# Performance work log

Hardware: AMD Instinct MI355X
Metric: run time of the kernel (lower is better)

Reference implementation:

```python
import jax, jax.numpy as jnp
import numpy as np

B, L, D, H = 8, 4096, 512, 8
DK = D // H
FACTOR = 5


def setup_inputs() -> dict:
    key = jax.random.key(0)
    ks = jax.random.split(key, 11)
    s = 0.02
    w = lambda k: (jax.random.normal(k, (D, D), jnp.float32) * s)
    b = lambda k: (jax.random.normal(k, (D,), jnp.float32) * s)
    return {
        "q": jax.random.normal(ks[0], (B, L, D), jnp.float32),
        "k": jax.random.normal(ks[1], (B, L, D), jnp.float32),
        "v": jax.random.normal(ks[2], (B, L, D), jnp.float32),
        "Wq": w(ks[3]), "bq": b(ks[4]),
        "Wk": w(ks[5]), "bk": b(ks[6]),
        "Wv": w(ks[7]), "bv": b(ks[8]),
        "Wo": w(ks[9]), "bo": b(ks[10]),
    }


def _autocorrelation(q, k, v, Wq, bq, Wk, bk, Wv, bv, Wo, bo):
    # projections -> [B, H, L, DK]
    def proj(x, W, bias):
        return (x @ W + bias).reshape(B, L, H, DK).transpose(0, 2, 1, 3)

    Q = proj(q, Wq, bq)
    K = proj(k, Wk, bk)
    V = proj(v, Wv, bv)

    # FFT-based autocorrelation along length dim
    Qf = jnp.fft.rfft(Q, axis=2)
    Kf = jnp.fft.rfft(K, axis=2)
    R = jnp.fft.irfft(Qf * jnp.conj(Kf), n=L, axis=2)  # [B, H, L, DK]

    # NOTE: this repo reduces over head then LENGTH, so topk runs over channel dim
    mean_value = R.mean(axis=(1, 2))          # [B, DK]
    mean_across_batch = mean_value.mean(axis=0)  # [DK]

    top_k = max(1, min(int(FACTOR * np.log(L)), L))
    actual_k = min(top_k, DK)                  # static: 41
    _, idx = jax.lax.top_k(mean_across_batch, actual_k)  # [k] channel-indices used as delays

    weights = jax.nn.softmax(mean_value[:, idx], axis=-1)  # [B, k]

    # top-k delay aggregation: sum_i roll(V, -idx_i, axis=2) * w_i
    t = jnp.arange(L)

    def body(acc, inp):
        d, wb = inp  # scalar delay, [B] weights
        pattern = jnp.take(V, (t + d) % L, axis=2)  # circular roll by -d
        return acc + pattern * wb[:, None, None, None], None

    agg, _ = jax.lax.scan(body, jnp.zeros_like(V), (idx, weights.T))

    out = agg.transpose(0, 2, 1, 3).reshape(B, L, D) @ Wo + bo
    return out


def reference(q, k, v, Wq, bq, Wk, bk, Wv, bv, Wo, bo):
    return _autocorrelation(q, k, v, Wq, bq, Wk, bk, Wv, bv, Wo, bo)
```

## Files before the change

kernel.cpp:

```cpp
#include <hip/hip_runtime.h>
#include <hip/hip_bf16.h>

#define LL 4096
#define DD 512
#define BB 8
#define KSEL 41

typedef __attribute__((ext_vector_type(4))) float f32x4;
typedef __attribute__((ext_vector_type(8))) short short8;

__device__ __forceinline__ ushort f2bf(float x) {
  __hip_bfloat16 h = __float2bfloat16(x);
  return *reinterpret_cast<ushort*>(&h);
}

__device__ __forceinline__ void g2lds16(const void* g, void* l) {
  __builtin_amdgcn_global_load_lds(
      (const __attribute__((address_space(1))) unsigned int*)g,
      (__attribute__((address_space(3))) unsigned int*)l, 16, 0, 0);
}

__global__ __launch_bounds__(512) void k_colsum(const float* __restrict__ q,
                                                const float* __restrict__ kk,
                                                float* __restrict__ qpart,
                                                float* __restrict__ kpart) {
  int lc = blockIdx.x, b = blockIdx.y, which = blockIdx.z;
  const float* src = which ? kk : q;
  float* part = which ? kpart : qpart;
  int lane = threadIdx.x & 63, w = threadIdx.x >> 6;
  int c8 = lane * 8;
  const float* p = src + ((size_t)b * LL + (size_t)lc * 256 + w * 32) * DD + c8;
  float a0 = 0, a1 = 0, a2 = 0, a3 = 0, a4 = 0, a5 = 0, a6 = 0, a7 = 0;
#pragma unroll 8
  for (int l = 0; l < 32; ++l) {
    f32x4 x = __builtin_nontemporal_load((const f32x4*)(p + (size_t)l * DD));
    f32x4 y = __builtin_nontemporal_load((const f32x4*)(p + (size_t)l * DD + 4));
    a0 += x[0]; a1 += x[1]; a2 += x[2]; a3 += x[3];
    a4 += y[0]; a5 += y[1]; a6 += y[2]; a7 += y[3];
  }
  float* dst = &part[((size_t)b * 128 + lc * 8 + w) * DD + c8];
  f32x4 o0 = {a0, a1, a2, a3}, o1 = {a4, a5, a6, a7};
  *(f32x4*)dst = o0;
  *(f32x4*)(dst + 4) = o1;
}

__global__ __launch_bounds__(256) void k_projw(
    const float* __restrict__ qpart, const float* __restrict__ kpart,
    const float* __restrict__ Wq, const float* __restrict__ Wk,
    const float* __restrict__ bv, const float* __restrict__ Wo,
    const float* __restrict__ Wv,
    float* __restrict__ partQ, float* __restrict__ partK,
    float* __restrict__ partO, ushort* __restrict__ WT) {
  __shared__ float ss[BB][64];
  __shared__ float wv[8][512];
  int bid = blockIdx.x;
  int tid = threadIdx.x;

  if (bid < 24) {
    int jc = bid & 7, which = bid >> 3;
    int j0 = jc * 64;
    if (which == 2) {
      float a0 = 0.f, a1 = 0.f;
      for (int j = 0; j < 64; ++j) {
        float b = bv[j0 + j];
        a0 += b * Wo[(size_t)(j0 + j) * DD + tid];
        a1 += b * Wo[(size_t)(j0 + j) * DD + tid + 256];
      }
      partO[(size_t)jc * DD + tid] = a0;
      partO[(size_t)jc * DD + tid + 256] = a1;
      return;
    }
    const float* part_in = which ? kpart : qpart;
    const float* W = which ? Wk : Wq;
    for (int e = tid; e < BB * 64; e += 256) {
      int b = e >> 6, j = e & 63;
      float s = 0.f;
#pragma unroll 8
      for (int p = 0; p < 128; ++p)
        s += part_in[((size_t)b * 128 + p) * DD + j0 + j];
      ss[b][j] = s;
    }
    __syncthreads();
    float a[BB][2];
#pragma unroll
    for (int b = 0; b < BB; ++b) { a[b][0] = 0.f; a[b][1] = 0.f; }
    for (int j = 0; j < 64; ++j) {
      float w0 = W[(size_t)(j0 + j) * DD + tid];
      float w1 = W[(size_t)(j0 + j) * DD + tid + 256];
#pragma unroll
      for (int b = 0; b < BB; ++b) {
        float sv = ss[b][j];
        a[b][0] += sv * w0;
        a[b][1] += sv * w1;
      }
    }
    float* part = which ? partK : partQ;
#pragma unroll
    for (int b = 0; b < BB; ++b) {
      part[((size_t)jc * BB + b) * DD + tid] = a[b][0];
      part[((size_t)jc * BB + b) * DD + tid + 256] = a[b][1];
    }
    return;
  }

  int b2 = bid - 24;
  int cb = b2 & 1, jg = b2 >> 1;
  int c = cb * 256 + tid;
  int j0 = jg * 8;
  for (int t = tid; t < 8 * 512; t += 256)
    wv[t >> 9][t & 511] = Wv[(size_t)(j0 + (t >> 9)) * DD + (t & 511)];
  __syncthreads();
  float acc[8] = {0, 0, 0, 0, 0, 0, 0, 0};
  for (int m = 0; m < DD; ++m) {
    float wo = Wo[(size_t)m * DD + c];
#pragma unroll
    for (int j = 0; j < 8; ++j) acc[j] += wv[j][m] * wo;
  }
  ushort4 o0, o1;
  o0.x = f2bf(acc[0]); o0.y = f2bf(acc[1]); o0.z = f2bf(acc[2]); o0.w = f2bf(acc[3]);
  o1.x = f2bf(acc[4]); o1.y = f2bf(acc[5]); o1.z = f2bf(acc[6]); o1.w = f2bf(acc[7]);
  *(ushort4*)&WT[(size_t)c * DD + j0] = o0;
  *(ushort4*)&WT[(size_t)c * DD + j0 + 4] = o1;
}

__global__ __launch_bounds__(512) void k_stats2(
    const float* __restrict__ partQ, const float* __restrict__ partK,
    const float* __restrict__ partO,
    const float* __restrict__ bq, const float* __restrict__ bk,
    const float* __restrict__ bo,
    int* __restrict__ idx_out, float* __restrict__ wts_out,
    float* __restrict__ bvo_out) {
  __shared__ float Sq[BB][DD];
  __shared__ float Sk[BB][DD];
  __shared__ float mvs[BB][64];
  __shared__ float mab[64];
  __shared__ int idxs[64];
  int tid = threadIdx.x;
  float bqv = bq[tid] * (float)LL, bkv = bk[tid] * (float)LL;
#pragma unroll
  for (int b = 0; b < BB; ++b) {
    float aq = 0.f, ak = 0.f;
#pragma unroll
    for (int jc = 0; jc < 8; ++jc) {
      aq += partQ[((size_t)jc * BB + b) * DD + tid];
      ak += partK[((size_t)jc * BB + b) * DD + tid];
    }
    Sq[b][tid] = aq + bqv;
    Sk[b][tid] = ak + bkv;
  }
  {
    float ao = 0.f;
#pragma unroll
    for (int jc = 0; jc < 8; ++jc) ao += partO[(size_t)jc * DD + tid];
    bvo_out[tid] = ao + bo[tid];
  }
  __syncthreads();
  {
    int b = tid >> 6, d = tid & 63;
    float s = 0.f;
#pragma unroll
    for (int h = 0; h < 8; ++h) s += Sq[b][h * 64 + d] * Sk[b][h * 64 + d];
    mvs[b][d] = s * (1.0f / ((float)LL * 8.0f));
  }
  __syncthreads();
  if (tid < 64) {
    float s = 0.f;
#pragma unroll
    for (int b = 0; b < BB; ++b) s += mvs[b][tid];
    mab[tid] = s * 0.125f;
  }
  __syncthreads();
  if (tid < 64) {
    float x = mab[tid];
    int r = 0;
    for (int d = 0; d < 64; ++d) {
      float y = mab[d];
      r += (y > x || (y == x && d < tid)) ? 1 : 0;
    }
    if (r < KSEL) { idxs[r] = tid; idx_out[r] = tid; }
  }
  __syncthreads();
  if (tid < BB) {
    int b = tid;
    float mx = -3.4e38f;
    for (int i = 0; i < KSEL; ++i) mx = fmaxf(mx, mvs[b][idxs[i]]);
    float s = 0.f;
    for (int i = 0; i < KSEL; ++i) s += expf(mvs[b][idxs[i]] - mx);
    float inv = 1.f / s;
    for (int i = 0; i < KSEL; ++i) wts_out[b * 64 + i] = expf(mvs[b][idxs[i]] - mx) * inv;
  }
}

__global__ __launch_bounds__(256) void k_conv(const float* __restrict__ v,
                                              const int* __restrict__ idx,
                                              const float* __restrict__ wts,
                                              ushort* __restrict__ vagg) {
  __shared__ ushort vwinT[128 * 136];
  __shared__ ushort Mlds[64 * 136];
  __shared__ float coefw[256];
  int lt = blockIdx.x;
  int ch0 = blockIdx.y * 128;
  int b = blockIdx.z;
  int tid = threadIdx.x;
  int l0 = lt * 64;

  coefw[tid] = 0.f;
  __syncthreads();
  if (tid < KSEL) coefw[64 + idx[tid]] = wts[b * 64 + tid];
  __syncthreads();

  {
    int c = tid & 127;
    int jh = tid >> 7;
    const float* vb = v + (size_t)b * LL * DD + ch0 + c;
#pragma unroll
    for (int it = 0; it < 8; ++it) {
      int j0 = (it * 2 + jh) * 8;
      union { unsigned int u[4]; short8 s; } pk;
#pragma unroll
      for (int p = 0; p < 4; ++p) {
        int ja = (l0 + j0 + 2 * p) & (LL - 1);
        int jb = (l0 + j0 + 2 * p + 1) & (LL - 1);
        float lo = vb[(size_t)ja * DD];
        float hi = vb[(size_t)jb * DD];
        pk.u[p] = (unsigned)f2bf(lo) | ((unsigned)f2bf(hi) << 16);
      }
      *(short8*)&vwinT[c * 136 + j0] = pk.s;
    }
  }
#pragma unroll
  for (int it = 0; it < 8; ++it) {
    int e = (it * 256 + tid) * 4;
    int r = e >> 7, j0 = e & 127;
    ushort4 m4;
    m4.x = f2bf(coefw[64 + j0 + 0 - r]);
    m4.y = f2bf(coefw[64 + j0 + 1 - r]);
    m4.z = f2bf(coefw[64 + j0 + 2 - r]);
    m4.w = f2bf(coefw[64 + j0 + 3 - r]);
    *(ushort4*)&Mlds[r * 136 + j0] = m4;
  }
  __syncthreads();

  int lane = tid & 63, w = tid >> 6;
  int r15 = lane & 15, g = lane >> 4;
  f32x4 acc[4][2] = {};
#pragma unroll
  for (int ks = 0; ks < 4; ++ks) {
    int kc = ks * 4 + g;
    short8 av[4], bvv[2];
#pragma unroll
    for (int m = 0; m < 4; ++m)
      av[m] = *(const short8*)&Mlds[(m * 16 + r15) * 136 + kc * 8];
#pragma unroll
    for (int n = 0; n < 2; ++n)
      bvv[n] = *(const short8*)&vwinT[(w * 32 + n * 16 + r15) * 136 + kc * 8];
#pragma unroll
    for (int m = 0; m < 4; ++m)
#pragma unroll
      for (int n = 0; n < 2; ++n)
        acc[m][n] = __builtin_amdgcn_mfma_f32_16x16x32_bf16(av[m], bvv[n], acc[m][n], 0, 0, 0);
  }

  ushort* vout = vagg + ((size_t)b * LL + l0) * DD + ch0;
#pragma unroll
  for (int m = 0; m < 4; ++m)
#pragma unroll
    for (int n = 0; n < 2; ++n)
#pragma unroll
      for (int r = 0; r < 4; ++r) {
        int row = m * 16 + g * 4 + r;
        int col = w * 32 + n * 16 + r15;
        vout[(size_t)row * DD + col] = f2bf(acc[m][n][r]);
      }
}

__global__ __launch_bounds__(256) void k_gemm(const ushort* __restrict__ A,
                                              const ushort* __restrict__ BT,
                                              const float* __restrict__ bias,
                                              float* __restrict__ C) {
  __shared__ ushort lA[128 * 64];
  __shared__ ushort lB[128 * 64];
  int bcol = blockIdx.x * 128;
  int brow = blockIdx.y * 128;
  int tid = threadIdx.x;
  int lane = tid & 63, wid = tid >> 6;
  int wr = wid >> 1, wc = wid & 1;
  int r15 = lane & 15, g = lane >> 4;
  f32x4 acc[4][4] = {};
  for (int k0 = 0; k0 < DD; k0 += 64) {
#pragma unroll
    for (int it = 0; it < 4; ++it) {
      int ch = it * 256 + tid;
      int row = ch >> 3;
      int clg = (ch & 7) ^ (row & 7);
      g2lds16(A + (size_t)(brow + row) * DD + k0 + clg * 8, &lA[ch * 8]);
      g2lds16(BT + (size_t)(bcol + row) * DD + k0 + clg * 8, &lB[ch * 8]);
    }
    asm volatile("s_waitcnt vmcnt(0)" ::: "memory");
    __syncthreads();
#pragma unroll
    for (int ks = 0; ks < 2; ++ks) {
      int kc = ks * 4 + g;
      short8 av[4], bv[4];
#pragma unroll
      for (int m = 0; m < 4; ++m) {
        int row = wr * 64 + m * 16 + r15;
        av[m] = *(const short8*)&lA[(row * 8 + (kc ^ (row & 7))) * 8];
        int col = wc * 64 + m * 16 + r15;
        bv[m] = *(const short8*)&lB[(col * 8 + (kc ^ (col & 7))) * 8];
      }
#pragma unroll
      for (int m = 0; m < 4; ++m)
#pragma unroll
        for (int n = 0; n < 4; ++n)
          acc[m][n] = __builtin_amdgcn_mfma_f32_16x16x32_bf16(av[m], bv[n], acc[m][n], 0, 0, 0);
    }
    __syncthreads();
  }
#pragma unroll
  for (int n = 0; n < 4; ++n) {
    int col = bcol + wc * 64 + n * 16 + r15;
    float bc = bias[col];
#pragma unroll
    for (int m = 0; m < 4; ++m) {
      int row = brow + wr * 64 + m * 16 + g * 4;
#pragma unroll
      for (int r = 0; r < 4; ++r)
        C[(size_t)(row + r) * DD + col] = acc[m][n][r] + bc;
    }
  }
}

extern "C" void kernel_launch(void* const* d_in, const int* in_sizes, int n_in,
                              void* d_out, int out_size, void* d_ws, size_t ws_size,
                              hipStream_t stream) {
  const float* q  = (const float*)d_in[0];
  const float* k  = (const float*)d_in[1];
  const float* v  = (const float*)d_in[2];
  const float* Wq = (const float*)d_in[3];
  const float* bq = (const float*)d_in[4];
  const float* Wk = (const float*)d_in[5];
  const float* bk = (const float*)d_in[6];
  const float* Wv = (const float*)d_in[7];
  const float* bv = (const float*)d_in[8];
  const float* Wo = (const float*)d_in[9];
  const float* bo = (const float*)d_in[10];
  float* out = (float*)d_out;

  char* ws = (char*)d_ws;
  ushort* vagg  = (ushort*)(ws + 0x0);
  ushort* wvot  = (ushort*)(ws + 0x2100000);
  int*   idx    = (int*)(ws + 0x2388800);
  float* wts    = (float*)(ws + 0x2388900);
  float* bvo    = (float*)(ws + 0x2389100);
  float* qpart  = (float*)(ws + 0x0);
  float* kpart  = (float*)(ws + 0x200000);
  float* partQ  = (float*)(ws + 0x2180000);
  float* partK  = (float*)(ws + 0x21A0000);
  float* partO  = (float*)(ws + 0x21C0000);

  k_colsum<<<dim3(16, 8, 2), 512, 0, stream>>>(q, k, qpart, kpart);
  k_projw<<<dim3(152), 256, 0, stream>>>(qpart, kpart, Wq, Wk, bv, Wo, Wv,
                                         partQ, partK, partO, wvot);
  k_stats2<<<dim3(1), 512, 0, stream>>>(partQ, partK, partO, bq, bk, bo, idx, wts, bvo);
  k_conv<<<dim3(64, 4, 8), 256, 0, stream>>>(v, idx, wts, vagg);
  k_gemm<<<dim3(4, 256), 256, 0, stream>>>(vagg, wvot, bvo, out);
}
```

Baseline: 129.1 us.

## Project V by WvWo before delay aggregation and fuse with column sums

Uses the fact that the circular delay aggregation is linear, so it commutes with the per-row projection. The projection V·(Wv·Wo) now runs first as a bf16 MFMA GEMM, fused into one launch with the q/k column-sum blocks. The shift-and-weight convolution then works on the projected bf16 P and writes the final fp32 output with the bias, which removes the separate output GEMM and the vagg round-trip. The trade-off is an extra bf16 intermediate P that must be written and re-read, and the column-sum layout changes to 32 partials per batch.

```diff
diff --git a/kernel.cpp b/kernel.cpp
--- a/kernel.cpp
+++ b/kernel.cpp
@@ -20,16 +20,116 @@
       (__attribute__((address_space(3))) unsigned int*)l, 16, 0, 0);
 }
 
-__global__ __launch_bounds__(512) void k_colsum(const float* __restrict__ q,
-                                                const float* __restrict__ kk,
-                                                float* __restrict__ qpart,
-                                                float* __restrict__ kpart) {
-  int lc = blockIdx.x, b = blockIdx.y, which = blockIdx.z;
+__global__ __launch_bounds__(256) void k_wvot(const float* __restrict__ Wv,
+                                              const float* __restrict__ Wo,
+                                              ushort* __restrict__ WT) {
+  __shared__ float wv[8][512];
+  int tid = threadIdx.x;
+  int c = blockIdx.x * 256 + tid;
+  int j0 = blockIdx.y * 8;
+  for (int t = tid; t < 8 * 512; t += 256)
+    wv[t >> 9][t & 511] = Wv[(size_t)(j0 + (t >> 9)) * DD + (t & 511)];
+  __syncthreads();
+  float acc[8] = {0, 0, 0, 0, 0, 0, 0, 0};
+  for (int m = 0; m < DD; ++m) {
+    float wo = Wo[(size_t)m * DD + c];
+#pragma unroll
+    for (int j = 0; j < 8; ++j) acc[j] += wv[j][m] * wo;
+  }
+  ushort4 o0, o1;
+  o0.x = f2bf(acc[0]); o0.y = f2bf(acc[1]); o0.z = f2bf(acc[2]); o0.w = f2bf(acc[3]);
+  o1.x = f2bf(acc[4]); o1.y = f2bf(acc[5]); o1.z = f2bf(acc[6]); o1.w = f2bf(acc[7]);
+  *(ushort4*)&WT[(size_t)c * DD + j0] = o0;
+  *(ushort4*)&WT[(size_t)c * DD + j0 + 4] = o1;
+}
+
+union SmemF {
+  struct { ushort lA[128 * 64]; ushort lB[128 * 64]; } g;
+  float red[4][512];
+};
+
+__global__ __launch_bounds__(256) void k_fused(
+    const float* __restrict__ q, const float* __restrict__ kk,
+    const float* __restrict__ v, const ushort* __restrict__ WvoT,
+    ushort* __restrict__ P, float* __restrict__ qpart, float* __restrict__ kpart) {
+  __shared__ SmemF sm;
+  int bid = blockIdx.x;
+  int tid = threadIdx.x;
+
+  if (bid < 1024) {
+    int bcol = (bid & 3) * 128;
+    int brow = ((bid >> 2) & 31) * 128;
+    int b = bid >> 7;
+    const float* vb = v + (size_t)b * LL * DD;
+    int lane = tid & 63, wid = tid >> 6;
+    int wr = wid >> 1, wc = wid & 1;
+    int r15 = lane & 15, g = lane >> 4;
+    f32x4 acc[4][4] = {};
+    for (int k0 = 0; k0 < DD; k0 += 64) {
+#pragma unroll
+      for (int it = 0; it < 4; ++it) {
+        int e = it * 256 + tid;
+        int row = e >> 3, chl = e & 7;
+        const float* src = vb + (size_t)(brow + row) * DD + k0 + ((chl ^ (row & 7)) * 8);
+        f32x4 x = *(const f32x4*)src;
+        f32x4 y = *(const f32x4*)(src + 4);
+        union { ushort us[8]; short8 s; } pk;
+        pk.us[0] = f2bf(x[0]); pk.us[1] = f2bf(x[1]);
+        pk.us[2] = f2bf(x[2]); pk.us[3] = f2bf(x[3]);
+        pk.us[4] = f2bf(y[0]); pk.us[5] = f2bf(y[1]);
+        pk.us[6] = f2bf(y[2]); pk.us[7] = f2bf(y[3]);
+        *(short8*)&sm.g.lA[e * 8] = pk.s;
+      }
+#pragma unroll
+      for (int it = 0; it < 4; ++it) {
+        int ch = it * 256 + tid;
+        int row = ch >> 3;
+        int clg = (ch & 7) ^ (row & 7);
+        g2lds16(WvoT + (size_t)(bcol + row) * DD + k0 + clg * 8, &sm.g.lB[ch * 8]);
+      }
+      asm volatile("s_waitcnt vmcnt(0)" ::: "memory");
+      __syncthreads();
+#pragma unroll
+      for (int ks = 0; ks < 2; ++ks) {
+        int kc = ks * 4 + g;
+        short8 av[4], bv[4];
+#pragma unroll
+        for (int m = 0; m < 4; ++m) {
+          int row = wr * 64 + m * 16 + r15;
+          av[m] = *(const short8*)&sm.g.lA[(row * 8 + (kc ^ (row & 7))) * 8];
+          int col = wc * 64 + m * 16 + r15;
+          bv[m] = *(const short8*)&sm.g.lB[(col * 8 + (kc ^ (col & 7))) * 8];
+        }
+#pragma unroll
+        for (int m = 0; m < 4; ++m)
+#pragma unroll
+          for (int n = 0; n < 4; ++n)
+            acc[m][n] = __builtin_amdgcn_mfma_f32_16x16x32_bf16(av[m], bv[n], acc[m][n], 0, 0, 0);
+      }
+      __syncthreads();
+    }
+    ushort* Pb = P + ((size_t)b * LL + brow) * DD + bcol;
+#pragma unroll
+    for (int n = 0; n < 4; ++n) {
+      int col = wc * 64 + n * 16 + r15;
+#pragma unroll
+      for (int m = 0; m < 4; ++m) {
+        int row = wr * 64 + m * 16 + g * 4;
+#pragma unroll
+        for (int r = 0; r < 4; ++r)
+          Pb[(size_t)(row + r) * DD + col] = f2bf(acc[m][n][r]);
+      }
+    }
+    return;
+  }
+
+  int cbid = bid - 1024;
+  int which = cbid & 1, lc = (cbid >> 1) & 31, b = cbid >> 6;
   const float* src = which ? kk : q;
   float* part = which ? kpart : qpart;
-  int lane = threadIdx.x & 63, w = threadIdx.x >> 6;
+  int lane = tid & 63, w = tid >> 6;
   int c8 = lane * 8;
-  const float* p = src + ((size_t)b * LL + (size_t)lc * 256 + w * 32) * DD + c8;
+  const float* p = src + ((size_t)b * LL + (size_t)lc * 128 + w * 32) * DD + c8;
   float a0 = 0, a1 = 0, a2 = 0, a3 = 0, a4 = 0, a5 = 0, a6 = 0, a7 = 0;
 #pragma unroll 8
   for (int l = 0; l < 32; ++l) {
@@ -38,89 +138,70 @@
     a0 += x[0]; a1 += x[1]; a2 += x[2]; a3 += x[3];
     a4 += y[0]; a5 += y[1]; a6 += y[2]; a7 += y[3];
   }
-  float* dst = &part[((size_t)b * 128 + lc * 8 + w) * DD + c8];
   f32x4 o0 = {a0, a1, a2, a3}, o1 = {a4, a5, a6, a7};
-  *(f32x4*)dst = o0;
-  *(f32x4*)(dst + 4) = o1;
-}
-
-__global__ __launch_bounds__(256) void k_projw(
+  *(f32x4*)&sm.red[w][c8] = o0;
+  *(f32x4*)&sm.red[w][c8 + 4] = o1;
+  __syncthreads();
+#pragma unroll
+  for (int t = 0; t < 2; ++t) {
+    int c = tid * 2 + t;
+    float s = sm.red[0][c] + sm.red[1][c] + sm.red[2][c] + sm.red[3][c];
+    part[((size_t)b * 32 + lc) * DD + c] = s;
+  }
+}
+
+__global__ __launch_bounds__(256) void k_proj(
     const float* __restrict__ qpart, const float* __restrict__ kpart,
     const float* __restrict__ Wq, const float* __restrict__ Wk,
     const float* __restrict__ bv, const float* __restrict__ Wo,
-    const float* __restrict__ Wv,
     float* __restrict__ partQ, float* __restrict__ partK,
-    float* __restrict__ partO, ushort* __restrict__ WT) {
+    float* __restrict__ partO) {
   __shared__ float ss[BB][64];
-  __shared__ float wv[8][512];
   int bid = blockIdx.x;
   int tid = threadIdx.x;
-
-  if (bid < 24) {
-    int jc = bid & 7, which = bid >> 3;
-    int j0 = jc * 64;
-    if (which == 2) {
-      float a0 = 0.f, a1 = 0.f;
-      for (int j = 0; j < 64; ++j) {
-        float b = bv[j0 + j];
-        a0 += b * Wo[(size_t)(j0 + j) * DD + tid];
-        a1 += b * Wo[(size_t)(j0 + j) * DD + tid + 256];
-      }
-      partO[(size_t)jc * DD + tid] = a0;
-      partO[(size_t)jc * DD + tid + 256] = a1;
-      return;
-    }
-    const float* part_in = which ? kpart : qpart;
-    const float* W = which ? Wk : Wq;
-    for (int e = tid; e < BB * 64; e += 256) {
-      int b = e >> 6, j = e & 63;
-      float s = 0.f;
+  int jc = bid & 7, which = bid >> 3;
+  int j0 = jc * 64;
+  if (which == 2) {
+    float a0 = 0.f, a1 = 0.f;
+    for (int j = 0; j < 64; ++j) {
+      float b = bv[j0 + j];
+      a0 += b * Wo[(size_t)(j0 + j) * DD + tid];
+      a1 += b * Wo[(size_t)(j0 + j) * DD + tid + 256];
+    }
+    partO[(size_t)jc * DD + tid] = a0;
+    partO[(size_t)jc * DD + tid + 256] = a1;
+    return;
+  }
+  const float* part_in = which ? kpart : qpart;
+  const float* W = which ? Wk : Wq;
+  for (int e = tid; e < BB * 64; e += 256) {
+    int b = e >> 6, j = e & 63;
+    float s = 0.f;
 #pragma unroll 8
-      for (int p = 0; p < 128; ++p)
-        s += part_in[((size_t)b * 128 + p) * DD + j0 + j];
-      ss[b][j] = s;
-    }
-    __syncthreads();
-    float a[BB][2];
-#pragma unroll
-    for (int b = 0; b < BB; ++b) { a[b][0] = 0.f; a[b][1] = 0.f; }
-    for (int j = 0; j < 64; ++j) {
-      float w0 = W[(size_t)(j0 + j) * DD + tid];
-      float w1 = W[(size_t)(j0 + j) * DD + tid + 256];
-#pragma unroll
-      for (int b = 0; b < BB; ++b) {
-        float sv = ss[b][j];
-        a[b][0] += sv * w0;
-        a[b][1] += sv * w1;
-      }
-    }
-    float* part = which ? partK : partQ;
+    for (int p = 0; p < 32; ++p)
+      s += part_in[((size_t)b * 32 + p) * DD + j0 + j];
+    ss[b][j] = s;
+  }
+  __syncthreads();
+  float a[BB][2];
+#pragma unroll
+  for (int b = 0; b < BB; ++b) { a[b][0] = 0.f; a[b][1] = 0.f; }
+  for (int j = 0; j < 64; ++j) {
+    float w0 = W[(size_t)(j0 + j) * DD + tid];
+    float w1 = W[(size_t)(j0 + j) * DD + tid + 256];
 #pragma unroll
     for (int b = 0; b < BB; ++b) {
-      part[((size_t)jc * BB + b) * DD + tid] = a[b][0];
-      part[((size_t)jc * BB + b) * DD + tid + 256] = a[b][1];
-    }
-    return;
-  }
-
-  int b2 = bid - 24;
-  int cb = b2 & 1, jg = b2 >> 1;
-  int c = cb * 256 + tid;
-  int j0 = jg * 8;
-  for (int t = tid; t < 8 * 512; t += 256)
-    wv[t >> 9][t & 511] = Wv[(size_t)(j0 + (t >> 9)) * DD + (t & 511)];
-  __syncthreads();
-  float acc[8] = {0, 0, 0, 0, 0, 0, 0, 0};
-  for (int m = 0; m < DD; ++m) {
-    float wo = Wo[(size_t)m * DD + c];
-#pragma unroll
-    for (int j = 0; j < 8; ++j) acc[j] += wv[j][m] * wo;
-  }
-  ushort4 o0, o1;
-  o0.x = f2bf(acc[0]); o0.y = f2bf(acc[1]); o0.z = f2bf(acc[2]); o0.w = f2bf(acc[3]);
-  o1.x = f2bf(acc[4]); o1.y = f2bf(acc[5]); o1.z = f2bf(acc[6]); o1.w = f2bf(acc[7]);
-  *(ushort4*)&WT[(size_t)c * DD + j0] = o0;
-  *(ushort4*)&WT[(size_t)c * DD + j0 + 4] = o1;
+      float sv = ss[b][j];
+      a[b][0] += sv * w0;
+      a[b][1] += sv * w1;
+    }
+  }
+  float* part = which ? partK : partQ;
+#pragma unroll
+  for (int b = 0; b < BB; ++b) {
+    part[((size_t)jc * BB + b) * DD + tid] = a[b][0];
+    part[((size_t)jc * BB + b) * DD + tid + 256] = a[b][1];
+  }
 }
 
 __global__ __launch_bounds__(512) void k_stats2(
@@ -191,11 +272,12 @@
   }
 }
 
-__global__ __launch_bounds__(256) void k_conv(const float* __restrict__ v,
-                                              const int* __restrict__ idx,
-                                              const float* __restrict__ wts,
-                                              ushort* __restrict__ vagg) {
-  __shared__ ushort vwinT[128 * 136];
+__global__ __launch_bounds__(256) void k_convp(const ushort* __restrict__ P,
+                                               const int* __restrict__ idx,
+                                               const float* __restrict__ wts,
+                                               const float* __restrict__ bvo,
+                                               float* __restrict__ C) {
+  __shared__ ushort pwinT[128 * 136];
   __shared__ ushort Mlds[64 * 136];
   __shared__ float coefw[256];
   int lt = blockIdx.x;
@@ -210,22 +292,25 @@
   __syncthreads();
 
   {
-    int c = tid & 127;
-    int jh = tid >> 7;
-    const float* vb = v + (size_t)b * LL * DD + ch0 + c;
-#pragma unroll
-    for (int it = 0; it < 8; ++it) {
-      int j0 = (it * 2 + jh) * 8;
-      union { unsigned int u[4]; short8 s; } pk;
-#pragma unroll
-      for (int p = 0; p < 4; ++p) {
-        int ja = (l0 + j0 + 2 * p) & (LL - 1);
-        int jb = (l0 + j0 + 2 * p + 1) & (LL - 1);
-        float lo = vb[(size_t)ja * DD];
-        float hi = vb[(size_t)jb * DD];
-        pk.u[p] = (unsigned)f2bf(lo) | ((unsigned)f2bf(hi) << 16);
-      }
-      *(short8*)&vwinT[c * 136 + j0] = pk.s;
+    int c2 = (tid & 63) * 2;
+    int jh = tid >> 6;
+    const ushort* Pb = P + (size_t)b * LL * DD + ch0 + c2;
+    unsigned int pk[32];
+#pragma unroll
+    for (int jj = 0; jj < 32; ++jj) {
+      int ja = (l0 + jh * 32 + jj) & (LL - 1);
+      pk[jj] = *(const unsigned int*)&Pb[(size_t)ja * DD];
+    }
+#pragma unroll
+    for (int qq = 0; qq < 4; ++qq) {
+      union { ushort us[8]; short8 s; } lo, hi;
+#pragma unroll
+      for (int i = 0; i < 8; ++i) {
+        lo.us[i] = (ushort)(pk[qq * 8 + i] & 0xffffu);
+        hi.us[i] = (ushort)(pk[qq * 8 + i] >> 16);
+      }
+      *(short8*)&pwinT[c2 * 136 + jh * 32 + qq * 8] = lo.s;
+      *(short8*)&pwinT[(c2 + 1) * 136 + jh * 32 + qq * 8] = hi.s;
     }
   }
 #pragma unroll
@@ -253,7 +338,7 @@
       av[m] = *(const short8*)&Mlds[(m * 16 + r15) * 136 + kc * 8];
 #pragma unroll
     for (int n = 0; n < 2; ++n)
-      bvv[n] = *(const short8*)&vwinT[(w * 32 + n * 16 + r15) * 136 + kc * 8];
+      bvv[n] = *(const short8*)&pwinT[(w * 32 + n * 16 + r15) * 136 + kc * 8];
 #pragma unroll
     for (int m = 0; m < 4; ++m)
 #pragma unroll
@@ -261,72 +346,17 @@
         acc[m][n] = __builtin_amdgcn_mfma_f32_16x16x32_bf16(av[m], bvv[n], acc[m][n], 0, 0, 0);
   }
 
-  ushort* vout = vagg + ((size_t)b * LL + l0) * DD + ch0;
-#pragma unroll
-  for (int m = 0; m < 4; ++m)
-#pragma unroll
-    for (int n = 0; n < 2; ++n)
-#pragma unroll
-      for (int r = 0; r < 4; ++r) {
-        int row = m * 16 + g * 4 + r;
-        int col = w * 32 + n * 16 + r15;
-        vout[(size_t)row * DD + col] = f2bf(acc[m][n][r]);
-      }
-}
-
-__global__ __launch_bounds__(256) void k_gemm(const ushort* __restrict__ A,
-                                              const ushort* __restrict__ BT,
-                                              const float* __restrict__ bias,
-                                              float* __restrict__ C) {
-  __shared__ ushort lA[128 * 64];
-  __shared__ ushort lB[128 * 64];
-  int bcol = blockIdx.x * 128;
-  int brow = blockIdx.y * 128;
-  int tid = threadIdx.x;
-  int lane = tid & 63, wid = tid >> 6;
-  int wr = wid >> 1, wc = wid & 1;
-  int r15 = lane & 15, g = lane >> 4;
-  f32x4 acc[4][4] = {};
-  for (int k0 = 0; k0 < DD; k0 += 64) {
-#pragma unroll
-    for (int it = 0; it < 4; ++it) {
-      int ch = it * 256 + tid;
-      int row = ch >> 3;
-      int clg = (ch & 7) ^ (row & 7);
-      g2lds16(A + (size_t)(brow + row) * DD + k0 + clg * 8, &lA[ch * 8]);
-      g2lds16(BT + (size_t)(bcol + row) * DD + k0 + clg * 8, &lB[ch * 8]);
-    }
-    asm volatile("s_waitcnt vmcnt(0)" ::: "memory");
-    __syncthreads();
-#pragma unroll
-    for (int ks = 0; ks < 2; ++ks) {
-      int kc = ks * 4 + g;
-      short8 av[4], bv[4];
-#pragma unroll
-      for (int m = 0; m < 4; ++m) {
-        int row = wr * 64 + m * 16 + r15;
-        av[m] = *(const short8*)&lA[(row * 8 + (kc ^ (row & 7))) * 8];
-        int col = wc * 64 + m * 16 + r15;
-        bv[m] = *(const short8*)&lB[(col * 8 + (kc ^ (col & 7))) * 8];
-      }
-#pragma unroll
-      for (int m = 0; m < 4; ++m)
-#pragma unroll
-        for (int n = 0; n < 4; ++n)
-          acc[m][n] = __builtin_amdgcn_mfma_f32_16x16x32_bf16(av[m], bv[n], acc[m][n], 0, 0, 0);
-    }
-    __syncthreads();
-  }
-#pragma unroll
-  for (int n = 0; n < 4; ++n) {
-    int col = bcol + wc * 64 + n * 16 + r15;
-    float bc = bias[col];
+  float* Cb = C + ((size_t)b * LL + l0) * DD + ch0;
+#pragma unroll
+  for (int n = 0; n < 2; ++n) {
+    int col = w * 32 + n * 16 + r15;
+    float bc = bvo[ch0 + col];
 #pragma unroll
     for (int m = 0; m < 4; ++m) {
-      int row = brow + wr * 64 + m * 16 + g * 4;
+      int row = m * 16 + g * 4;
 #pragma unroll
       for (int r = 0; r < 4; ++r)
-        C[(size_t)(row + r) * DD + col] = acc[m][n][r] + bc;
+        Cb[(size_t)(row + r) * DD + col] = acc[m][n][r] + bc;
     }
   }
 }
@@ -348,21 +378,20 @@
   float* out = (float*)d_out;
 
   char* ws = (char*)d_ws;
-  ushort* vagg  = (ushort*)(ws + 0x0);
-  ushort* wvot  = (ushort*)(ws + 0x2100000);
-  int*   idx    = (int*)(ws + 0x2388800);
-  float* wts    = (float*)(ws + 0x2388900);
-  float* bvo    = (float*)(ws + 0x2389100);
-  float* qpart  = (float*)(ws + 0x0);
-  float* kpart  = (float*)(ws + 0x200000);
+  ushort* P     = (ushort*)(ws + 0x0);
+  ushort* wvot  = (ushort*)(ws + 0x2000000);
+  float* qpart  = (float*)(ws + 0x2080000);
+  float* kpart  = (float*)(ws + 0x2100000);
   float* partQ  = (float*)(ws + 0x2180000);
   float* partK  = (float*)(ws + 0x21A0000);
   float* partO  = (float*)(ws + 0x21C0000);
-
-  k_colsum<<<dim3(16, 8, 2), 512, 0, stream>>>(q, k, qpart, kpart);
-  k_projw<<<dim3(152), 256, 0, stream>>>(qpart, kpart, Wq, Wk, bv, Wo, Wv,
-                                         partQ, partK, partO, wvot);
+  int*   idx    = (int*)(ws + 0x21C8000);
+  float* wts    = (float*)(ws + 0x21C9000);
+  float* bvo    = (float*)(ws + 0x21CA000);
+
+  k_wvot<<<dim3(2, 64), 256, 0, stream>>>(Wv, Wo, wvot);
+  k_fused<<<dim3(1536), 256, 0, stream>>>(q, k, v, wvot, P, qpart, kpart);
+  k_proj<<<dim3(24), 256, 0, stream>>>(qpart, kpart, Wq, Wk, bv, Wo, partQ, partK, partO);
   k_stats2<<<dim3(1), 512, 0, stream>>>(partQ, partK, partO, bq, bk, bo, idx, wts, bvo);
-  k_conv<<<dim3(64, 4, 8), 256, 0, stream>>>(v, idx, wts, vagg);
-  k_gemm<<<dim3(4, 256), 256, 0, stream>>>(vagg, wvot, bvo, out);
-}
+  k_convp<<<dim3(64, 4, 8), 256, 0, stream>>>(P, idx, wts, bvo, out);
+}
```

Result: slower. 162.7 us (+26.1%).
